# Kernel tuning notes

Hardware: AMD Instinct MI355X
Metric: run time of the kernel (lower is better)

## Reference

```python
import jax, jax.numpy as jnp
import numpy as np

K = 2  # shift stride from module init


def setup_inputs() -> dict:
    key = jax.random.key(0)
    k1, k2, k3 = jax.random.split(key, 3)
    # x: [B, C, D, H, W] dense volumetric features
    x = jax.random.normal(k1, (2, 128, 48, 48, 48), dtype=jnp.float32)
    # 1x1x1 Conv3d weight [out_channels, 2*in_channels] (kernel dims squeezed) + bias
    W = jax.random.normal(k2, (128, 256), dtype=jnp.float32) * 0.02
    b = jax.random.normal(k3, (128,), dtype=jnp.float32) * 0.02
    return {"x": x, "W": W, "b": b}


def _max_relative(x):
    # torch.cat([x[..., -i:], x[..., :-i]], dim=ax) == roll by +i along ax
    B, C, D, H, Wd = x.shape
    xj = jnp.zeros_like(x)  # x - x
    for axis, n in ((2, D), (3, H), (4, Wd)):
        for i in range(K, n, K):  # static shift schedule, fine under jit
            xj = jnp.maximum(xj, x - jnp.roll(x, i, axis=axis))
    return xj


def reference(x, W, b):
    xj = _max_relative(x)
    y = jnp.concatenate([x, xj], axis=1)  # [B, 2C, D, H, W]
    # 1x1x1 conv == channel GEMM
    out = jnp.einsum('bcdhw,oc->bodhw', y, W) + b[None, :, None, None, None]
    return jax.nn.relu(out)
```

## Files before the change

kernel.cpp:

```cpp
#include <hip/hip_runtime.h>
#include <hip/hip_bf16.h>

#define SVOL 110592
#define HD   2304
#define NDIM 48

typedef __attribute__((ext_vector_type(4))) float f32x4;
typedef __attribute__((ext_vector_type(8))) short bf16x8;
typedef __attribute__((ext_vector_type(2))) unsigned int u32x2;
typedef unsigned short ushort_t;
typedef unsigned int uint_t;

__device__ __forceinline__ ushort_t f2b(float f) {
    __hip_bfloat16 h = __float2bfloat16(f);
    return *(ushort_t*)&h;
}
__device__ __forceinline__ float b2f(uint_t u) {
    union { float f; uint_t i; } v; v.i = u << 16; return v.f;
}

__global__ __launch_bounds__(256) void wconv_kernel(const float* __restrict__ W,
                                                    ushort_t* __restrict__ Wb) {
    int i = blockIdx.x * 256 + threadIdx.x;
    Wb[i] = f2b(W[i]);
}

__global__ __launch_bounds__(256) void tables_kernel(const float* __restrict__ x,
                                                     ushort_t* __restrict__ tabDp,
                                                     ushort_t* __restrict__ tabH,
                                                     ushort_t* __restrict__ tabW) {
    __shared__ __align__(16) float sl[4 * HD];
    const int bc   = blockIdx.x;
    const int part = blockIdx.y;
    const float* __restrict__ xp = x + (size_t)bc * SVOL + (size_t)part * 16 * HD;
    const int t    = threadIdx.x;
    const int w4   = t >> 6;
    const int lane = t & 63;
    const int dlh  = t / NDIM;
    const int wh   = t - dlh * NDIM;

    f32x4 accD[3][2];
    #pragma unroll
    for (int s = 0; s < 3; ++s)
        #pragma unroll
        for (int p = 0; p < 2; ++p)
            #pragma unroll
            for (int e = 0; e < 4; ++e) accD[s][p][e] = 3e38f;

    for (int q = 0; q < 4; ++q) {
        const float* __restrict__ qp = xp + (size_t)q * 4 * HD;
        #pragma unroll
        for (int k = 0; k < 9; ++k) {
            const int i16 = (k * 4 + w4) * 64 + lane;
            __builtin_amdgcn_global_load_lds(
                (const __attribute__((address_space(1))) void*)(qp + (size_t)i16 * 4),
                (__attribute__((address_space(3))) void*)&sl[(k * 4 + w4) * 256],
                16, 0, 0);
        }
        __syncthreads();

        #pragma unroll
        for (int s = 0; s < 3; ++s) {
            const int j = t + s * 256;
            if (j < 576) {
                #pragma unroll
                for (int dl = 0; dl < 4; ++dl) {
                    f32x4 v = ((const f32x4*)sl)[dl * 576 + j];
                    #pragma unroll
                    for (int e = 0; e < 4; ++e)
                        accD[s][dl & 1][e] = fminf(accD[s][dl & 1][e], v[e]);
                }
            }
        }
        if (t < 192) {
            const int d = part * 16 + q * 4 + dlh;
            {
                const float* pb = sl + dlh * HD + wh;
                float m0 = 3e38f, m1 = 3e38f;
                #pragma unroll
                for (int h = 0; h < NDIM; h += 2) {
                    m0 = fminf(m0, pb[h * NDIM]);
                    m1 = fminf(m1, pb[(h + 1) * NDIM]);
                }
                tabH[(size_t)bc * 2 * HD + d * NDIM + wh]      = f2b(m0);
                tabH[(size_t)bc * 2 * HD + HD + d * NDIM + wh] = f2b(m1);
            }
            {
                const f32x4* pr = (const f32x4*)(sl + dlh * HD + wh * NDIM);
                const int rot = wh % 12;
                float m0 = 3e38f, m1 = 3e38f;
                #pragma unroll
                for (int j = 0; j < 12; ++j) {
                    int jj = j + rot; if (jj >= 12) jj -= 12;
                    f32x4 v = pr[jj];
                    m0 = fminf(m0, fminf(v[0], v[2]));
                    m1 = fminf(m1, fminf(v[1], v[3]));
                }
                tabW[(size_t)bc * 2 * HD + d * NDIM + wh]      = f2b(m0);
                tabW[(size_t)bc * 2 * HD + HD + d * NDIM + wh] = f2b(m1);
            }
        }
        __syncthreads();
    }

    ushort_t* tDo = tabDp + ((size_t)part * 256 + bc) * 2 * HD;
    #pragma unroll
    for (int s = 0; s < 3; ++s) {
        const int j = t + s * 256;
        if (j < 576) {
            union { ushort_t s4[4]; uint2 u; } p0, p1;
            #pragma unroll
            for (int e = 0; e < 4; ++e) { p0.s4[e] = f2b(accD[s][0][e]); p1.s4[e] = f2b(accD[s][1][e]); }
            *(uint2*)(tDo + j * 4)      = p0.u;
            *(uint2*)(tDo + HD + j * 4) = p1.u;
        }
    }
}

__global__ __launch_bounds__(256) void merge_kernel(const ushort_t* __restrict__ tabDp,
                                                    ushort_t* __restrict__ tabD) {
    const int i = blockIdx.x * 256 + threadIdx.x;
    const size_t off = (size_t)256 * 2 * HD / 4;
    union U { uint2 u; ushort_t s4[4]; } a, b1, c, o;
    a.u  = ((const uint2*)tabDp)[i];
    b1.u = ((const uint2*)tabDp)[i + off];
    c.u  = ((const uint2*)tabDp)[i + 2 * off];
    #pragma unroll
    for (int j = 0; j < 4; ++j)
        o.s4[j] = f2b(fminf(b2f(a.s4[j]), fminf(b2f(b1.s4[j]), b2f(c.s4[j]))));
    ((uint2*)tabD)[i] = o.u;
}

#define TPB 2
__global__ __launch_bounds__(256) void gemm_kernel(const float* __restrict__ x,
                                                   const ushort_t* __restrict__ tabD,
                                                   const ushort_t* __restrict__ tabH,
                                                   const ushort_t* __restrict__ tabW,
                                                   const ushort_t* __restrict__ Wb,
                                                   const float* __restrict__ bias,
                                                   float* __restrict__ out) {
    __shared__ __align__(1024) ushort_t ytile[16384];
    const int bx  = blockIdx.x;
    const int b   = blockIdx.y;
    const int swz = (bx & 7) * 108 + (bx >> 3);
    const int tile0 = swz * TPB;
    const int t  = threadIdx.x;
    const int wid = t >> 6, lane = t & 63;
    const int row  = lane & 3;
    const int colq = (lane >> 2) & 3;
    const int sqq  = (lane >> 4) & 3;
    const int sloc = (sqq * 4 + colq) * 4;
    const int l15 = lane & 15, l4 = lane >> 4;

    const float* __restrict__ xb = x + (size_t)b * 128 * SVOL;
    const size_t tbb = (size_t)b * 128 * 2 * HD;

    const ushort_t* wp = Wb + (size_t)(wid * 32 + l15) * 256 + l4 * 8;
    float bv[2];
    #pragma unroll
    for (int m = 0; m < 2; ++m) bv[m] = bias[wid * 32 + m * 16 + l15];

    const int d  = (tile0 * 64) / HD;
    const int rb = tile0 * 64 - d * HD;
    const int pd = d & 1;

    uint2 pk[8][2];
    auto stage = [&](int tile) {
        const int r  = rb + (tile - tile0) * 64 + sloc;
        const int h  = r / NDIM;
        const int w0 = r - h * NDIM;
        const int ph = h & 1;
        const int s  = d * HD + r;
        #pragma unroll
        for (int it = 0; it < 8; ++it) {
            const int c = (it * 4 + wid) * 4 + row;
            const size_t tb = tbb + (size_t)c * 2 * HD;
            f32x4 xv = *(const f32x4*)(xb + (size_t)c * SVOL + s);
            uint2 md2 = *(const uint2*)(tabD + tb + pd * HD + r);
            uint2 mh2 = *(const uint2*)(tabH + tb + ph * HD + d * NDIM + w0);
            const float mW0 = b2f(tabW[tb + d * NDIM + h]);
            const float mW1 = b2f(tabW[tb + HD + d * NDIM + h]);
            float mD[4] = { b2f(md2.x & 0xffffu), b2f(md2.x >> 16),
                            b2f(md2.y & 0xffffu), b2f(md2.y >> 16) };
            float mH[4] = { b2f(mh2.x & 0xffffu), b2f(mh2.x >> 16),
                            b2f(mh2.y & 0xffffu), b2f(mh2.y >> 16) };
            union { __hip_bfloat16 h4[4]; uint2 u; } ox, oj;
            #pragma unroll
            for (int j = 0; j < 4; ++j) {
                const float mm = fminf(mD[j], fminf(mH[j], (j & 1) ? mW1 : mW0));
                ox.h4[j] = __float2bfloat16(xv[j]);
                oj.h4[j] = __float2bfloat16(fmaxf(0.0f, xv[j] - mm));
            }
            pk[it][0] = ox.u; pk[it][1] = oj.u;
        }
    };

    const uint_t lds_base = (uint_t)(uintptr_t)(__attribute__((address_space(3))) ushort_t*)&ytile[0];
    float* ob = out + (size_t)b * 128 * SVOL;

    stage(tile0);

    #pragma unroll
    for (int tt = 0; tt < TPB; ++tt) {
        __syncthreads();
        {
            #pragma unroll
            for (int it = 0; it < 8; ++it) {
                const int A = (it * 4 + wid) * 512 + sqq * 128 + row * 32 + colq * 8;
                *(uint2*)&ytile[A >> 1]             = pk[it][0];
                *(uint2*)&ytile[(A + 16384) >> 1]   = pk[it][1];
            }
        }
        __syncthreads();

        const uint_t addrB = lds_base + (uint_t)(l4 * 1024 + l15 * 8);
        f32x4 acc[4][2] = {};
        #pragma unroll
        for (int ph4 = 0; ph4 < 4; ++ph4) {
            u32x2 lo[2][4], hi[2][4];
            #pragma unroll
            for (int kk = 0; kk < 2; ++kk)
                #pragma unroll
                for (int n = 0; n < 4; ++n) {
                    const uint_t ad = addrB + (uint_t)((ph4 * 2 + kk) * 4096 + n * 128);
                    asm volatile("ds_read_b64_tr_b16 %0, %2 offset:0\n\t"
                                 "ds_read_b64_tr_b16 %1, %2 offset:512"
                                 : "=&v"(lo[kk][n]), "=&v"(hi[kk][n]) : "v"(ad) : "memory");
                }
            asm volatile("s_waitcnt lgkmcnt(0)" ::: "memory");
            __builtin_amdgcn_sched_barrier(0);
            #pragma unroll
            for (int kk = 0; kk < 2; ++kk) {
                bf16x8 aw[2];
                #pragma unroll
                for (int m = 0; m < 2; ++m)
                    aw[m] = *(const bf16x8*)(wp + ((size_t)m * 16 * 256 + (ph4 * 2 + kk) * 32));
                #pragma unroll
                for (int n = 0; n < 4; ++n) {
                    union { u32x2 u2[2]; bf16x8 v; } cvt;
                    cvt.u2[0] = lo[kk][n]; cvt.u2[1] = hi[kk][n];
                    #pragma unroll
                    for (int m = 0; m < 2; ++m)
                        acc[n][m] = __builtin_amdgcn_mfma_f32_16x16x32_bf16(cvt.v, aw[m], acc[n][m], 0, 0, 0);
                }
            }
        }

        if (tt + 1 < TPB) stage(tile0 + tt + 1);

        const int s_b = (tile0 + tt) * 64;
        #pragma unroll
        for (int n = 0; n < 4; ++n)
            #pragma unroll
            for (int m = 0; m < 2; ++m) {
                const int o = wid * 32 + m * 16 + l15;
                const int s = s_b + n * 16 + l4 * 4;
                f32x4 r;
                #pragma unroll
                for (int j = 0; j < 4; ++j) r[j] = fmaxf(acc[n][m][j] + bv[m], 0.0f);
                *(f32x4*)(ob + (size_t)o * SVOL + s) = r;
            }
    }
}

extern "C" void kernel_launch(void* const* d_in, const int* in_sizes, int n_in,
                              void* d_out, int out_size, void* d_ws, size_t ws_size,
                              hipStream_t stream) {
    const float* x    = (const float*)d_in[0];
    const float* W    = (const float*)d_in[1];
    const float* bias = (const float*)d_in[2];
    float* out = (float*)d_out;

    ushort_t* Wb    = (ushort_t*)d_ws;
    ushort_t* tabDp = (ushort_t*)((char*)d_ws + 65536);
    ushort_t* tabH  = tabDp + (size_t)3 * 256 * 2 * HD;
    ushort_t* tabW  = tabH  + (size_t)256 * 2 * HD;
    ushort_t* tabD  = tabW  + (size_t)256 * 2 * HD;

    wconv_kernel<<<128, 256, 0, stream>>>(W, Wb);
    tables_kernel<<<dim3(256, 3), 256, 0, stream>>>(x, tabDp, tabH, tabW);
    merge_kernel<<<1152, 256, 0, stream>>>(tabDp, tabD);
    gemm_kernel<<<dim3(864, 2), 256, 0, stream>>>(x, tabD, tabH, tabW, Wb, bias, out);
}
```

Measured before the change: 113.2 us.

## Restructure GEMM so each wave owns 16 spatial columns, removing block barriers

The GEMM kernel now processes one 64-voxel tile per block instead of two. Each wave stages, transposes and multiplies its own 16-voxel slice across all 128 output channels using wave-private LDS, so the block-wide __syncthreads calls and the cross-tile software pipelining are gone. The grid doubles to keep coverage. In exchange, each wave reloads every weight fragment (8x8 bf16x8 loads from global/L2) with no reuse across waves, and there is no longer any overlap of the next tile's loads with compute.

```diff
diff --git a/kernel.cpp b/kernel.cpp
--- a/kernel.cpp
+++ b/kernel.cpp
@@ -131,7 +131,6 @@
     ((uint2*)tabD)[i] = o.u;
 }
 
-#define TPB 2
 __global__ __launch_bounds__(256) void gemm_kernel(const float* __restrict__ x,
                                                    const ushort_t* __restrict__ tabD,
                                                    const ushort_t* __restrict__ tabH,
@@ -139,127 +138,92 @@
                                                    const ushort_t* __restrict__ Wb,
                                                    const float* __restrict__ bias,
                                                    float* __restrict__ out) {
-    __shared__ __align__(1024) ushort_t ytile[16384];
+    __shared__ __align__(1024) ushort_t ytile[4 * 4096];
     const int bx  = blockIdx.x;
     const int b   = blockIdx.y;
-    const int swz = (bx & 7) * 108 + (bx >> 3);
-    const int tile0 = swz * TPB;
-    const int t  = threadIdx.x;
+    const int swz = (bx & 7) * 216 + (bx >> 3);
+    const int t   = threadIdx.x;
     const int wid = t >> 6, lane = t & 63;
-    const int row  = lane & 3;
-    const int colq = (lane >> 2) & 3;
-    const int sqq  = (lane >> 4) & 3;
-    const int sloc = (sqq * 4 + colq) * 4;
+    const int s4   = lane & 3;
+    const int cgrp = lane >> 2;
     const int l15 = lane & 15, l4 = lane >> 4;
+
+    const int d  = (swz * 64) / HD;
+    const int rb = swz * 64 - d * HD;
+    const int pd = d & 1;
+    const int r_t = rb + wid * 16 + s4 * 4;
+    const int h   = r_t / NDIM;
+    const int w0  = r_t - h * NDIM;
+    const int ph  = h & 1;
+    const int sg  = d * HD + r_t;
 
     const float* __restrict__ xb = x + (size_t)b * 128 * SVOL;
     const size_t tbb = (size_t)b * 128 * 2 * HD;
 
-    const ushort_t* wp = Wb + (size_t)(wid * 32 + l15) * 256 + l4 * 8;
-    float bv[2];
-    #pragma unroll
-    for (int m = 0; m < 2; ++m) bv[m] = bias[wid * 32 + m * 16 + l15];
-
-    const int d  = (tile0 * 64) / HD;
-    const int rb = tile0 * 64 - d * HD;
-    const int pd = d & 1;
-
-    uint2 pk[8][2];
-    auto stage = [&](int tile) {
-        const int r  = rb + (tile - tile0) * 64 + sloc;
-        const int h  = r / NDIM;
-        const int w0 = r - h * NDIM;
-        const int ph = h & 1;
-        const int s  = d * HD + r;
-        #pragma unroll
-        for (int it = 0; it < 8; ++it) {
-            const int c = (it * 4 + wid) * 4 + row;
-            const size_t tb = tbb + (size_t)c * 2 * HD;
-            f32x4 xv = *(const f32x4*)(xb + (size_t)c * SVOL + s);
-            uint2 md2 = *(const uint2*)(tabD + tb + pd * HD + r);
-            uint2 mh2 = *(const uint2*)(tabH + tb + ph * HD + d * NDIM + w0);
-            const float mW0 = b2f(tabW[tb + d * NDIM + h]);
-            const float mW1 = b2f(tabW[tb + HD + d * NDIM + h]);
-            float mD[4] = { b2f(md2.x & 0xffffu), b2f(md2.x >> 16),
-                            b2f(md2.y & 0xffffu), b2f(md2.y >> 16) };
-            float mH[4] = { b2f(mh2.x & 0xffffu), b2f(mh2.x >> 16),
-                            b2f(mh2.y & 0xffffu), b2f(mh2.y >> 16) };
-            union { __hip_bfloat16 h4[4]; uint2 u; } ox, oj;
-            #pragma unroll
-            for (int j = 0; j < 4; ++j) {
-                const float mm = fminf(mD[j], fminf(mH[j], (j & 1) ? mW1 : mW0));
-                ox.h4[j] = __float2bfloat16(xv[j]);
-                oj.h4[j] = __float2bfloat16(fmaxf(0.0f, xv[j] - mm));
-            }
-            pk[it][0] = ox.u; pk[it][1] = oj.u;
-        }
-    };
-
-    const uint_t lds_base = (uint_t)(uintptr_t)(__attribute__((address_space(3))) ushort_t*)&ytile[0];
+    ushort_t* q = &ytile[wid * 4096];
+    #pragma unroll
+    for (int it = 0; it < 8; ++it) {
+        const int c = it * 16 + cgrp;
+        const size_t tb = tbb + (size_t)c * 2 * HD;
+        f32x4 xv  = *(const f32x4*)(xb + (size_t)c * SVOL + sg);
+        uint2 md2 = *(const uint2*)(tabD + tb + (size_t)pd * HD + r_t);
+        uint2 mh2 = *(const uint2*)(tabH + tb + (size_t)ph * HD + d * NDIM + w0);
+        const float mW0 = b2f(tabW[tb + d * NDIM + h]);
+        const float mW1 = b2f(tabW[tb + HD + d * NDIM + h]);
+        float mD[4] = { b2f(md2.x & 0xffffu), b2f(md2.x >> 16),
+                        b2f(md2.y & 0xffffu), b2f(md2.y >> 16) };
+        float mH[4] = { b2f(mh2.x & 0xffffu), b2f(mh2.x >> 16),
+                        b2f(mh2.y & 0xffffu), b2f(mh2.y >> 16) };
+        union { __hip_bfloat16 h4[4]; uint2 u; } ox, oj;
+        #pragma unroll
+        for (int j = 0; j < 4; ++j) {
+            const float mm = fminf(mD[j], fminf(mH[j], (j & 1) ? mW1 : mW0));
+            ox.h4[j] = __float2bfloat16(xv[j]);
+            oj.h4[j] = __float2bfloat16(fmaxf(0.0f, xv[j] - mm));
+        }
+        const int aoff = (c >> 2) * 64 + (c & 3) * 16 + s4 * 4;
+        *(uint2*)&q[aoff]        = ox.u;
+        *(uint2*)&q[aoff + 2048] = oj.u;
+    }
+    asm volatile("s_waitcnt lgkmcnt(0)" ::: "memory");
+    __builtin_amdgcn_sched_barrier(0);
+
+    const uint_t qbyte = (uint_t)(uintptr_t)(__attribute__((address_space(3))) ushort_t*)&ytile[0]
+                       + (uint_t)(wid * 8192 + l4 * 256 + l15 * 8);
+    u32x2 lo[8], hi[8];
+    #pragma unroll
+    for (int kk = 0; kk < 8; ++kk) {
+        const uint_t ad = qbyte + (uint_t)(kk * 1024);
+        asm volatile("ds_read_b64_tr_b16 %0, %2 offset:0\n\t"
+                     "ds_read_b64_tr_b16 %1, %2 offset:128"
+                     : "=&v"(lo[kk]), "=&v"(hi[kk]) : "v"(ad) : "memory");
+    }
+    asm volatile("s_waitcnt lgkmcnt(0)" ::: "memory");
+    __builtin_amdgcn_sched_barrier(0);
+
+    const ushort_t* __restrict__ wp = Wb + (size_t)l15 * 256 + l4 * 8;
+    f32x4 acc[8] = {};
+    #pragma unroll
+    for (int kk = 0; kk < 8; ++kk) {
+        union { u32x2 u2[2]; bf16x8 v; } cvt;
+        cvt.u2[0] = lo[kk]; cvt.u2[1] = hi[kk];
+        #pragma unroll
+        for (int m = 0; m < 8; ++m) {
+            bf16x8 aw = *(const bf16x8*)(wp + ((size_t)m * 16 * 256 + kk * 32));
+            acc[m] = __builtin_amdgcn_mfma_f32_16x16x32_bf16(cvt.v, aw, acc[m], 0, 0, 0);
+        }
+    }
+
     float* ob = out + (size_t)b * 128 * SVOL;
-
-    stage(tile0);
-
-    #pragma unroll
-    for (int tt = 0; tt < TPB; ++tt) {
-        __syncthreads();
-        {
-            #pragma unroll
-            for (int it = 0; it < 8; ++it) {
-                const int A = (it * 4 + wid) * 512 + sqq * 128 + row * 32 + colq * 8;
-                *(uint2*)&ytile[A >> 1]             = pk[it][0];
-                *(uint2*)&ytile[(A + 16384) >> 1]   = pk[it][1];
-            }
-        }
-        __syncthreads();
-
-        const uint_t addrB = lds_base + (uint_t)(l4 * 1024 + l15 * 8);
-        f32x4 acc[4][2] = {};
-        #pragma unroll
-        for (int ph4 = 0; ph4 < 4; ++ph4) {
-            u32x2 lo[2][4], hi[2][4];
-            #pragma unroll
-            for (int kk = 0; kk < 2; ++kk)
-                #pragma unroll
-                for (int n = 0; n < 4; ++n) {
-                    const uint_t ad = addrB + (uint_t)((ph4 * 2 + kk) * 4096 + n * 128);
-                    asm volatile("ds_read_b64_tr_b16 %0, %2 offset:0\n\t"
-                                 "ds_read_b64_tr_b16 %1, %2 offset:512"
-                                 : "=&v"(lo[kk][n]), "=&v"(hi[kk][n]) : "v"(ad) : "memory");
-                }
-            asm volatile("s_waitcnt lgkmcnt(0)" ::: "memory");
-            __builtin_amdgcn_sched_barrier(0);
-            #pragma unroll
-            for (int kk = 0; kk < 2; ++kk) {
-                bf16x8 aw[2];
-                #pragma unroll
-                for (int m = 0; m < 2; ++m)
-                    aw[m] = *(const bf16x8*)(wp + ((size_t)m * 16 * 256 + (ph4 * 2 + kk) * 32));
-                #pragma unroll
-                for (int n = 0; n < 4; ++n) {
-                    union { u32x2 u2[2]; bf16x8 v; } cvt;
-                    cvt.u2[0] = lo[kk][n]; cvt.u2[1] = hi[kk][n];
-                    #pragma unroll
-                    for (int m = 0; m < 2; ++m)
-                        acc[n][m] = __builtin_amdgcn_mfma_f32_16x16x32_bf16(cvt.v, aw[m], acc[n][m], 0, 0, 0);
-                }
-            }
-        }
-
-        if (tt + 1 < TPB) stage(tile0 + tt + 1);
-
-        const int s_b = (tile0 + tt) * 64;
-        #pragma unroll
-        for (int n = 0; n < 4; ++n)
-            #pragma unroll
-            for (int m = 0; m < 2; ++m) {
-                const int o = wid * 32 + m * 16 + l15;
-                const int s = s_b + n * 16 + l4 * 4;
-                f32x4 r;
-                #pragma unroll
-                for (int j = 0; j < 4; ++j) r[j] = fmaxf(acc[n][m][j] + bv[m], 0.0f);
-                *(f32x4*)(ob + (size_t)o * SVOL + s) = r;
-            }
+    const int s_st = d * HD + rb + wid * 16 + l4 * 4;
+    #pragma unroll
+    for (int m = 0; m < 8; ++m) {
+        const int o = m * 16 + l15;
+        const float bv = bias[o];
+        f32x4 r;
+        #pragma unroll
+        for (int j = 0; j < 4; ++j) r[j] = fmaxf(acc[m][j] + bv, 0.0f);
+        *(f32x4*)(ob + (size_t)o * SVOL + s_st) = r;
     }
 }
 
@@ -280,5 +244,5 @@
     wconv_kernel<<<128, 256, 0, stream>>>(W, Wb);
     tables_kernel<<<dim3(256, 3), 256, 0, stream>>>(x, tabDp, tabH, tabW);
     merge_kernel<<<1152, 256, 0, stream>>>(tabDp, tabD);
-    gemm_kernel<<<dim3(864, 2), 256, 0, stream>>>(x, tabD, tabH, tabW, Wb, bias, out);
-}
+    gemm_kernel<<<dim3(1728, 2), 256, 0, stream>>>(x, tabD, tabH, tabW, Wb, bias, out);
+}
```

Result: slower. 168.6 us (+48.9%).
